# Optimization experiments

Hardware: AMD Instinct MI355X
Metric: run time of the kernel (lower is better)

Reference implementation:

```python
import jax, jax.numpy as jnp
import numpy as np


def setup_inputs() -> dict:
    key = jax.random.key(0)
    k1, k2, k3, k4 = jax.random.split(key, 4)
    n, L, h = 512, 257, 256
    l = L - 1
    hidden, n_labels = 256, 50
    feat = jax.random.normal(k1, (n, L, h), dtype=jnp.float32)
    heads = jax.random.randint(k2, (n, l), 0, L, dtype=jnp.int64)
    masks = jnp.ones((n, l), dtype=jnp.float32)
    # torch nn.Linear layout: (out_features, in_features); xavier-normal-ish scale
    W1 = jax.random.normal(k3, (hidden, 2 * h), dtype=jnp.float32) * (2.0 / (hidden + 2 * h)) ** 0.5
    b1 = jnp.zeros((hidden,), dtype=jnp.float32)
    W2 = jax.random.normal(k4, (n_labels, hidden), dtype=jnp.float32) * (2.0 / (n_labels + hidden)) ** 0.5
    b2 = jnp.zeros((n_labels,), dtype=jnp.float32)
    return {"feat": feat, "heads": heads, "masks": masks,
            "W1": W1, "b1": b1, "W2": W2, "b2": b2}


def reference(feat, heads, masks, W1, b1, W2, b2):
    # feat: (n, L, h); heads: (n, l) with l = L-1, values in [0, L)
    dependent_f = feat[:, 1:, :]                                   # (n, l, h)
    # head_f[b, i] = feat[b, heads[b, i]]  (the gather)
    head_f = jnp.take_along_axis(feat, heads[:, :, None], axis=1)   # (n, l, h)
    cat_f = jnp.concatenate((dependent_f, head_f), axis=2)          # (n, l, 2h)
    hid = jax.nn.relu(jnp.einsum('nlh,oh->nlo', cat_f, W1) + b1)    # (n, l, hidden); dropout is identity at eval
    label_f = jnp.einsum('nlo,ko->nlk', hid, W2) + b2               # (n, l, n_labels)
    return label_f
```

## Files before the change

### kernel.cpp

```cpp
#include <hip/hip_runtime.h>
#include <hip/hip_bf16.h>
#include <stdint.h>

#define AS1 __attribute__((address_space(1)))
#define AS3 __attribute__((address_space(3)))

typedef __bf16 bf16x8 __attribute__((ext_vector_type(8)));
typedef __bf16 bf16x4 __attribute__((ext_vector_type(4)));
typedef float  floatx4 __attribute__((ext_vector_type(4)));

static constexpr int NB   = 512;
static constexpr int LL   = 257;
static constexpr int HH   = 256;
static constexpr int M    = NB * (LL - 1);
static constexpr int K1   = 2 * HH;
static constexpr int NHID = 256;
static constexpr int NLAB = 50;

__device__ __forceinline__ void async16(const void* gptr, void* ldsptr) {
  __builtin_amdgcn_global_load_lds((const AS1 void*)gptr, (AS3 void*)ldsptr, 16, 0, 0);
}

__global__ void prep_w(const float* __restrict__ W1, const float* __restrict__ W2,
                       __bf16* __restrict__ w1b, __bf16* __restrict__ w2b) {
  int idx = blockIdx.x * 256 + threadIdx.x;
  if (idx < 16384) {
    const float4* s = (const float4*)(W1 + (size_t)idx * 8);
    float4 a = s[0], b = s[1];
    bf16x8 v;
    v[0]=(__bf16)a.x; v[1]=(__bf16)a.y; v[2]=(__bf16)a.z; v[3]=(__bf16)a.w;
    v[4]=(__bf16)b.x; v[5]=(__bf16)b.y; v[6]=(__bf16)b.z; v[7]=(__bf16)b.w;
    *(bf16x8*)(w1b + (size_t)idx * 8) = v;
  } else {
    int j = idx - 16384;
    int row = j >> 5;
    int col = (j & 31) * 8;
    float4 a = {0.f,0.f,0.f,0.f}, b = {0.f,0.f,0.f,0.f};
    if (row < NLAB) {
      const float4* s = (const float4*)(W2 + (size_t)row * 256 + col);
      a = s[0]; b = s[1];
    }
    bf16x8 v;
    v[0]=(__bf16)a.x; v[1]=(__bf16)a.y; v[2]=(__bf16)a.z; v[3]=(__bf16)a.w;
    v[4]=(__bf16)b.x; v[5]=(__bf16)b.y; v[6]=(__bf16)b.z; v[7]=(__bf16)b.w;
    *(bf16x8*)(w2b + (size_t)j * 8) = v;
  }
}

__global__ __launch_bounds__(256, 2)
void fused_kernel(const float* __restrict__ feat, const int* __restrict__ heads,
                  const __bf16* __restrict__ w1b, const float* __restrict__ b1,
                  const __bf16* __restrict__ w2b, const float* __restrict__ b2,
                  float* __restrict__ out) {
  __shared__ __align__(16) char smem[65536];
  float*  catS = (float*)smem;
  __bf16* W1s  = (__bf16*)(smem + 8192);
  __bf16* hidS = (__bf16*)smem;
  __bf16* W2s  = (__bf16*)(smem + 32768);

  const int t    = threadIdx.x;
  const int w    = t >> 6;
  const int lane = t & 63;
  const int lr   = lane & 15;
  const int q    = lane >> 4;
  const int mBase = blockIdx.x * 64;

  #pragma unroll
  for (int i = 0; i < 8; ++i) {
    int c = t + i * 256;
    int row = c >> 5, p = c & 31;
    int g = p ^ (row & 7);
    *(bf16x8*)(W2s + row * 256 + p * 8) =
        *(const bf16x8*)(w2b + (size_t)row * 256 + g * 8);
  }

  const int r0  = t >> 3;
  const int gs  = (t & 7) ^ (r0 & 7);
  const int m0  = mBase + r0;
  const int m1  = m0 + 32;
  const float* bd0 = feat + ((size_t)((m0 >> 8) * LL + (m0 & 255) + 1)) * HH;
  const float* bh0 = feat + ((size_t)((m0 >> 8) * LL + heads[m0])) * HH;
  const float* bd1 = feat + ((size_t)((m1 >> 8) * LL + (m1 & 255) + 1)) * HH;
  const float* bh1 = feat + ((size_t)((m1 >> 8) * LL + heads[m1])) * HH;
  const int catOff = gs * 4;

  const int n0 = t >> 2;
  const int gw = ((t & 3) ^ ((n0 >> 1) & 3)) * 8;

  floatx4 acc[4][4];
  #pragma unroll
  for (int i = 0; i < 4; ++i)
    #pragma unroll
    for (int j = 0; j < 4; ++j)
      acc[i][j] = (floatx4){0.f, 0.f, 0.f, 0.f};

  const int posw = (q ^ ((lr >> 1) & 3)) * 8;
  const int pc0  = (2 * q) ^ (lr & 7);
  const int pc1  = pc0 ^ 1;

  for (int kt = 0; kt < 16; ++kt) {
    const int k0 = kt * 32;
    __syncthreads();
    {
      const float* s0 = (kt < 8) ? bd0 : bh0;
      const float* s1 = (kt < 8) ? bd1 : bh1;
      const int kk = k0 & 255;
      async16(s0 + kk + catOff, catS + t * 4);
      async16(s1 + kk + catOff, catS + (t + 256) * 4);
      const __bf16* wsrc = w1b + k0 + gw;
      async16(wsrc + (size_t)n0 * K1,         W1s + t * 8);
      async16(wsrc + (size_t)(n0 + 64) * K1,  W1s + (t + 256) * 8);
      async16(wsrc + (size_t)(n0 + 128) * K1, W1s + (t + 512) * 8);
      async16(wsrc + (size_t)(n0 + 192) * K1, W1s + (t + 768) * 8);
    }
    __syncthreads();

    bf16x8 af[4], bb[4];
    #pragma unroll
    for (int oi = 0; oi < 4; ++oi) {
      const int o = w * 64 + oi * 16 + lr;
      af[oi] = *(const bf16x8*)(W1s + o * 32 + posw);
    }
    #pragma unroll
    for (int mi = 0; mi < 4; ++mi) {
      const int m = mi * 16 + lr;
      float4 fa = *(const float4*)(catS + m * 32 + pc0 * 4);
      float4 fb = *(const float4*)(catS + m * 32 + pc1 * 4);
      bf16x8 vv;
      vv[0]=(__bf16)fa.x; vv[1]=(__bf16)fa.y; vv[2]=(__bf16)fa.z; vv[3]=(__bf16)fa.w;
      vv[4]=(__bf16)fb.x; vv[5]=(__bf16)fb.y; vv[6]=(__bf16)fb.z; vv[7]=(__bf16)fb.w;
      bb[mi] = vv;
    }
    #pragma unroll
    for (int oi = 0; oi < 4; ++oi)
      #pragma unroll
      for (int mi = 0; mi < 4; ++mi)
        acc[oi][mi] = __builtin_amdgcn_mfma_f32_16x16x32_bf16(af[oi], bb[mi], acc[oi][mi], 0, 0, 0);
  }

  __syncthreads();

  float4 biasv[4];
  #pragma unroll
  for (int oi = 0; oi < 4; ++oi)
    biasv[oi] = *(const float4*)(b1 + w * 64 + oi * 16 + q * 4);

  #pragma unroll
  for (int mi = 0; mi < 4; ++mi) {
    const int m = mi * 16 + lr;
    const int s = lr & 7;
    #pragma unroll
    for (int oi = 0; oi < 4; ++oi) {
      const int j = w * 8 + oi * 2 + (q >> 1);
      bf16x4 hv;
      const float* bp = (const float*)&biasv[oi];
      #pragma unroll
      for (int r = 0; r < 4; ++r) {
        float v = acc[oi][mi][r] + bp[r];
        v = v > 0.f ? v : 0.f;
        hv[r] = (__bf16)v;
      }
      *(bf16x4*)(hidS + m * 256 + ((j ^ s) << 3) + (q & 1) * 4) = hv;
    }
  }
  __syncthreads();

  floatx4 acc2[4];
  #pragma unroll
  for (int i = 0; i < 4; ++i) acc2[i] = (floatx4){0.f, 0.f, 0.f, 0.f};

  const int m2 = w * 16 + lr;
  const int s2 = lr & 7;
  #pragma unroll
  for (int kt2 = 0; kt2 < 8; ++kt2) {
    const int gc = kt2 * 4 + q;
    bf16x8 a2 = *(const bf16x8*)(hidS + m2 * 256 + ((gc ^ s2) << 3));
    #pragma unroll
    for (int ni = 0; ni < 4; ++ni) {
      const int n = ni * 16 + lr;
      bf16x8 b2f = *(const bf16x8*)(W2s + n * 256 + ((gc ^ (lr & 7)) << 3));
      acc2[ni] = __builtin_amdgcn_mfma_f32_16x16x32_bf16(a2, b2f, acc2[ni], 0, 0, 0);
    }
  }

  const int rowBase = mBase + w * 16 + q * 4;
  #pragma unroll
  for (int ni = 0; ni < 4; ++ni) {
    const int col = ni * 16 + lr;
    if (col < NLAB) {
      const float bias = b2[col];
      #pragma unroll
      for (int r = 0; r < 4; ++r)
        out[(size_t)(rowBase + r) * NLAB + col] = acc2[ni][r] + bias;
    }
  }
}

extern "C" void kernel_launch(void* const* d_in, const int* in_sizes, int n_in,
                              void* d_out, int out_size, void* d_ws, size_t ws_size,
                              hipStream_t stream) {
  const float* feat  = (const float*)d_in[0];
  const int*   heads = (const int*)d_in[1];
  const float* W1 = (const float*)d_in[3];
  const float* b1 = (const float*)d_in[4];
  const float* W2 = (const float*)d_in[5];
  const float* b2 = (const float*)d_in[6];
  float* out = (float*)d_out;

  __bf16* w1b = (__bf16*)d_ws;
  __bf16* w2b = w1b + 256 * 512;

  prep_w<<<72, 256, 0, stream>>>(W1, W2, w1b, w2b);
  fused_kernel<<<M / 64, 256, 0, stream>>>(feat, heads, w1b, b1, w2b, b2, out);
}
```

Baseline: 259.6 us.

## Halve LDS footprint: bf16 cat tile, W2 in registers, raise occupancy

Features are now loaded with plain global loads, converted to bf16 in registers and stored to a padded bf16 LDS tile, instead of async-copying fp32 into LDS and converting on read. W2 is no longer staged in LDS. Each wave keeps its 16 output columns of W2 in registers, and the second GEMM is re-split so each wave owns columns rather than rows. Shared memory drops from 64KB to 32KB and launch bounds move to 4 blocks per CU, aiming for more latency hiding. The trade-offs are losing the async global-to-LDS path for features, more register pressure, and the wave handling columns 48-63 wasting part of its work.

```diff
diff --git a/kernel.cpp b/kernel.cpp
--- a/kernel.cpp
+++ b/kernel.cpp
@@ -14,8 +14,8 @@
 static constexpr int HH   = 256;
 static constexpr int M    = NB * (LL - 1);
 static constexpr int K1   = 2 * HH;
-static constexpr int NHID = 256;
 static constexpr int NLAB = 50;
+static constexpr int CAT_RS = 40;
 
 __device__ __forceinline__ void async16(const void* gptr, void* ldsptr) {
   __builtin_amdgcn_global_load_lds((const AS1 void*)gptr, (AS3 void*)ldsptr, 16, 0, 0);
@@ -47,16 +47,15 @@
   }
 }
 
-__global__ __launch_bounds__(256, 2)
+__global__ __launch_bounds__(256, 4)
 void fused_kernel(const float* __restrict__ feat, const int* __restrict__ heads,
                   const __bf16* __restrict__ w1b, const float* __restrict__ b1,
                   const __bf16* __restrict__ w2b, const float* __restrict__ b2,
                   float* __restrict__ out) {
-  __shared__ __align__(16) char smem[65536];
-  float*  catS = (float*)smem;
-  __bf16* W1s  = (__bf16*)(smem + 8192);
+  __shared__ __align__(16) char smem[32768];
+  __bf16* catS = (__bf16*)smem;
+  __bf16* W1s  = (__bf16*)(smem + 5120);
   __bf16* hidS = (__bf16*)smem;
-  __bf16* W2s  = (__bf16*)(smem + 32768);
 
   const int t    = threadIdx.x;
   const int w    = t >> 6;
@@ -65,27 +64,16 @@
   const int q    = lane >> 4;
   const int mBase = blockIdx.x * 64;
 
-  #pragma unroll
-  for (int i = 0; i < 8; ++i) {
-    int c = t + i * 256;
-    int row = c >> 5, p = c & 31;
-    int g = p ^ (row & 7);
-    *(bf16x8*)(W2s + row * 256 + p * 8) =
-        *(const bf16x8*)(w2b + (size_t)row * 256 + g * 8);
-  }
+  const int r  = t >> 2;
+  const int cc = t & 3;
+  const int m  = mBase + r;
+  const int seq = m >> 8;
+  const float* depP  = feat + ((size_t)(seq * LL + (m & 255) + 1)) * HH + cc * 8;
+  const float* headP = feat + ((size_t)(seq * LL + heads[m])) * HH + cc * 8;
+  __bf16* catW = catS + r * CAT_RS + cc * 8;
 
-  const int r0  = t >> 3;
-  const int gs  = (t & 7) ^ (r0 & 7);
-  const int m0  = mBase + r0;
-  const int m1  = m0 + 32;
-  const float* bd0 = feat + ((size_t)((m0 >> 8) * LL + (m0 & 255) + 1)) * HH;
-  const float* bh0 = feat + ((size_t)((m0 >> 8) * LL + heads[m0])) * HH;
-  const float* bd1 = feat + ((size_t)((m1 >> 8) * LL + (m1 & 255) + 1)) * HH;
-  const float* bh1 = feat + ((size_t)((m1 >> 8) * LL + heads[m1])) * HH;
-  const int catOff = gs * 4;
-
-  const int n0 = t >> 2;
-  const int gw = ((t & 3) ^ ((n0 >> 1) & 3)) * 8;
+  const int gw = ((t & 3) ^ ((t >> 3) & 3)) * 8;
+  const __bf16* w1base = w1b + (size_t)(t >> 2) * K1 + gw;
 
   floatx4 acc[4][4];
   #pragma unroll
@@ -95,23 +83,23 @@
       acc[i][j] = (floatx4){0.f, 0.f, 0.f, 0.f};
 
   const int posw = (q ^ ((lr >> 1) & 3)) * 8;
-  const int pc0  = (2 * q) ^ (lr & 7);
-  const int pc1  = pc0 ^ 1;
 
   for (int kt = 0; kt < 16; ++kt) {
-    const int k0 = kt * 32;
     __syncthreads();
     {
-      const float* s0 = (kt < 8) ? bd0 : bh0;
-      const float* s1 = (kt < 8) ? bd1 : bh1;
-      const int kk = k0 & 255;
-      async16(s0 + kk + catOff, catS + t * 4);
-      async16(s1 + kk + catOff, catS + (t + 256) * 4);
-      const __bf16* wsrc = w1b + k0 + gw;
-      async16(wsrc + (size_t)n0 * K1,         W1s + t * 8);
-      async16(wsrc + (size_t)(n0 + 64) * K1,  W1s + (t + 256) * 8);
-      async16(wsrc + (size_t)(n0 + 128) * K1, W1s + (t + 512) * 8);
-      async16(wsrc + (size_t)(n0 + 192) * K1, W1s + (t + 768) * 8);
+      const float* src = (kt < 8) ? depP : headP;
+      const int kk = (kt & 7) * 32;
+      float4 g0 = *(const float4*)(src + kk);
+      float4 g1 = *(const float4*)(src + kk + 4);
+      const __bf16* ws = w1base + kt * 32;
+      async16(ws,                      W1s + t * 8);
+      async16(ws + (size_t)64  * K1,   W1s + (t + 256) * 8);
+      async16(ws + (size_t)128 * K1,   W1s + (t + 512) * 8);
+      async16(ws + (size_t)192 * K1,   W1s + (t + 768) * 8);
+      bf16x8 cv;
+      cv[0]=(__bf16)g0.x; cv[1]=(__bf16)g0.y; cv[2]=(__bf16)g0.z; cv[3]=(__bf16)g0.w;
+      cv[4]=(__bf16)g1.x; cv[5]=(__bf16)g1.y; cv[6]=(__bf16)g1.z; cv[7]=(__bf16)g1.w;
+      *(bf16x8*)catW = cv;
     }
     __syncthreads();
 
@@ -122,15 +110,8 @@
       af[oi] = *(const bf16x8*)(W1s + o * 32 + posw);
     }
     #pragma unroll
-    for (int mi = 0; mi < 4; ++mi) {
-      const int m = mi * 16 + lr;
-      float4 fa = *(const float4*)(catS + m * 32 + pc0 * 4);
-      float4 fb = *(const float4*)(catS + m * 32 + pc1 * 4);
-      bf16x8 vv;
-      vv[0]=(__bf16)fa.x; vv[1]=(__bf16)fa.y; vv[2]=(__bf16)fa.z; vv[3]=(__bf16)fa.w;
-      vv[4]=(__bf16)fb.x; vv[5]=(__bf16)fb.y; vv[6]=(__bf16)fb.z; vv[7]=(__bf16)fb.w;
-      bb[mi] = vv;
-    }
+    for (int mi = 0; mi < 4; ++mi)
+      bb[mi] = *(const bf16x8*)(catS + (mi * 16 + lr) * CAT_RS + q * 8);
     #pragma unroll
     for (int oi = 0; oi < 4; ++oi)
       #pragma unroll
@@ -140,6 +121,11 @@
 
   __syncthreads();
 
+  bf16x8 w2f[8];
+  #pragma unroll
+  for (int kt2 = 0; kt2 < 8; ++kt2)
+    w2f[kt2] = *(const bf16x8*)(w2b + (size_t)(w * 16 + lr) * 256 + kt2 * 32 + q * 8);
+
   float4 biasv[4];
   #pragma unroll
   for (int oi = 0; oi < 4; ++oi)
@@ -147,20 +133,20 @@
 
   #pragma unroll
   for (int mi = 0; mi < 4; ++mi) {
-    const int m = mi * 16 + lr;
-    const int s = lr & 7;
+    const int mr = mi * 16 + lr;
+    const int s  = lr & 7;
     #pragma unroll
     for (int oi = 0; oi < 4; ++oi) {
-      const int j = w * 8 + oi * 2 + (q >> 1);
+      const int cj = w * 8 + oi * 2 + (q >> 1);
       bf16x4 hv;
       const float* bp = (const float*)&biasv[oi];
       #pragma unroll
-      for (int r = 0; r < 4; ++r) {
-        float v = acc[oi][mi][r] + bp[r];
+      for (int rr = 0; rr < 4; ++rr) {
+        float v = acc[oi][mi][rr] + bp[rr];
         v = v > 0.f ? v : 0.f;
-        hv[r] = (__bf16)v;
+        hv[rr] = (__bf16)v;
       }
-      *(bf16x4*)(hidS + m * 256 + ((j ^ s) << 3) + (q & 1) * 4) = hv;
+      *(bf16x4*)(hidS + mr * 256 + ((cj ^ s) << 3) + (q & 1) * 4) = hv;
     }
   }
   __syncthreads();
@@ -169,29 +155,25 @@
   #pragma unroll
   for (int i = 0; i < 4; ++i) acc2[i] = (floatx4){0.f, 0.f, 0.f, 0.f};
 
-  const int m2 = w * 16 + lr;
-  const int s2 = lr & 7;
   #pragma unroll
   for (int kt2 = 0; kt2 < 8; ++kt2) {
-    const int gc = kt2 * 4 + q;
-    bf16x8 a2 = *(const bf16x8*)(hidS + m2 * 256 + ((gc ^ s2) << 3));
     #pragma unroll
-    for (int ni = 0; ni < 4; ++ni) {
-      const int n = ni * 16 + lr;
-      bf16x8 b2f = *(const bf16x8*)(W2s + n * 256 + ((gc ^ (lr & 7)) << 3));
-      acc2[ni] = __builtin_amdgcn_mfma_f32_16x16x32_bf16(a2, b2f, acc2[ni], 0, 0, 0);
+    for (int mi = 0; mi < 4; ++mi) {
+      const int gc = kt2 * 4 + q;
+      bf16x8 a2 = *(const bf16x8*)(hidS + (mi * 16 + lr) * 256 + ((gc ^ (lr & 7)) << 3));
+      acc2[mi] = __builtin_amdgcn_mfma_f32_16x16x32_bf16(a2, w2f[kt2], acc2[mi], 0, 0, 0);
     }
   }
 
-  const int rowBase = mBase + w * 16 + q * 4;
-  #pragma unroll
-  for (int ni = 0; ni < 4; ++ni) {
-    const int col = ni * 16 + lr;
-    if (col < NLAB) {
-      const float bias = b2[col];
+  const int col = w * 16 + lr;
+  if (col < NLAB) {
+    const float bias = b2[col];
+    #pragma unroll
+    for (int mi = 0; mi < 4; ++mi) {
+      const int rowBase = mBase + mi * 16 + q * 4;
       #pragma unroll
-      for (int r = 0; r < 4; ++r)
-        out[(size_t)(rowBase + r) * NLAB + col] = acc2[ni][r] + bias;
+      for (int rr = 0; rr < 4; ++rr)
+        out[(size_t)(rowBase + rr) * NLAB + col] = acc2[mi][rr] + bias;
     }
   }
 }
```

Result: no change. 261.1 us (+0.6%).
